# Performance work log

Measured on AMD Instinct MI355X. Metric: run time of the kernel, lower is better.

## Reference

```python
import jax, jax.numpy as jnp
import numpy as np

# dims
D_IN, D, H, HD = 1536, 256, 8, 32
DEPTH, FFN = 2, 1024
B, L = 1, 8191
NGRIDS, TILE = 256, 256
SEGMENTS = [1024, 2048, 4096, 8192, 16384]   # get_optimal_segment_length(32768, 256)
RATIOS = [1, 2, 4, 8, 16]                    # LongNet canonical dilation ratios
SCALE = HD ** -0.5


def setup_inputs() -> dict:
    key = jax.random.key(0)
    ks = jax.random.split(key, 16)
    w = lambda k, s: jax.random.normal(k, s, jnp.float32) * 0.02
    return {
        "x": jax.random.normal(ks[0], (B, L, D_IN), jnp.float32),
        "coords": jax.random.randint(ks[1], (B, L, 2), 0, NGRIDS * TILE, jnp.int32),
        "proj_w": w(ks[2], (D_IN, D)), "proj_b": jnp.zeros((D,), jnp.float32),
        "cls_tok": w(ks[3], (1, 1, D)),
        "Wq": w(ks[4], (DEPTH, D, D)), "Wk": w(ks[5], (DEPTH, D, D)),
        "Wv": w(ks[6], (DEPTH, D, D)), "Wo": w(ks[7], (DEPTH, D, D)),
        "bq": jnp.zeros((DEPTH, D), jnp.float32), "bk": jnp.zeros((DEPTH, D), jnp.float32),
        "bv": jnp.zeros((DEPTH, D), jnp.float32), "bo": jnp.zeros((DEPTH, D), jnp.float32),
        "ln1_g": jnp.ones((DEPTH, D), jnp.float32), "ln1_b": jnp.zeros((DEPTH, D), jnp.float32),
        "ln2_g": jnp.ones((DEPTH, D), jnp.float32), "ln2_b": jnp.zeros((DEPTH, D), jnp.float32),
        "W1": w(ks[8], (DEPTH, D, FFN)), "b1": jnp.zeros((DEPTH, FFN), jnp.float32),
        "W2": w(ks[9], (DEPTH, FFN, D)), "b2": jnp.zeros((DEPTH, D), jnp.float32),
        "enc_g": jnp.ones((D,), jnp.float32), "enc_b": jnp.zeros((D,), jnp.float32),
        "norm_g": jnp.ones((D,), jnp.float32), "norm_b": jnp.zeros((D,), jnp.float32),
    }


def _ln(x, g, b):
    mu = x.mean(-1, keepdims=True)
    v = ((x - mu) ** 2).mean(-1, keepdims=True)
    return (x - mu) * jax.lax.rsqrt(v + 1e-5) * g + b


def _pos_table():
    # MAE-style 2D sincos pos embed, row 0 = cls (zeros). [NGRIDS^2+1, D]
    g = jnp.arange(NGRIDS, dtype=jnp.float32)
    gw, gh = jnp.meshgrid(g, g)  # gw[i,j]=j, gh[i,j]=i; flatten index = i*NGRIDS + j
    def one(pos):
        omega = 1.0 / (10000.0 ** (jnp.arange(D // 4, dtype=jnp.float32) / (D // 4)))
        o = pos.reshape(-1)[:, None] * omega[None]
        return jnp.concatenate([jnp.sin(o), jnp.cos(o)], -1)
    tab = jnp.concatenate([one(gw), one(gh)], -1)
    return jnp.concatenate([jnp.zeros((1, D), jnp.float32), tab], 0)


def _dilated_attn(q, k, v):
    # q,k,v: [B,S,H,HD]. LongNet: per (segment w, dilation r) branch, sparse in-segment
    # attention on stride-r rows (head-dependent offset h%r), branches fused via their
    # softmax log-sum-exp weights.
    S = q.shape[1]
    hh = jnp.arange(H)[:, None]
    outs, lses = [], []
    for w, r in zip(SEGMENTS, RATIOS):
        n = (S + w - 1) // w
        Sp = n * w
        def seg(t):
            tp = jnp.pad(t, ((0, 0), (0, Sp - S), (0, 0), (0, 0)))
            return tp.reshape(B, n, w, H, HD).transpose(0, 1, 3, 2, 4)  # [B,n,H,w,HD]
        qs_, ks_, vs_ = seg(q), seg(k), seg(v)
        t = w // r
        idx = (hh % r) + r * jnp.arange(t)[None, :]                  # [H,t]
        qs = qs_[:, :, hh, idx]                                      # [B,n,H,t,HD]
        ks = ks_[:, :, hh, idx]
        vs = vs_[:, :, hh, idx]
        valid = (jnp.arange(n)[:, None, None] * w + idx[None]) < S   # [n,H,t]
        sc = jnp.einsum('bnhtd,bnhsd->bnhts', qs, ks) * SCALE
        sc = jnp.where(valid[None, :, :, None, :], sc, -1e9)
        m = sc.max(-1, keepdims=True)
        p = jnp.exp(sc - m)
        den = p.sum(-1, keepdims=True)
        o = jnp.einsum('bnhts,bnhsd->bnhtd', p, vs) / den
        lse = m[..., 0] + jnp.log(den[..., 0])                       # [B,n,H,t]
        fo = jnp.zeros((B, n, H, w, HD), q.dtype).at[:, :, hh, idx].set(o)
        fl = jnp.full((B, n, H, w), -1e30, q.dtype).at[:, :, hh, idx].set(lse)
        outs.append(fo.transpose(0, 1, 3, 2, 4).reshape(B, Sp, H, HD)[:, :S])
        lses.append(fl.transpose(0, 1, 3, 2).reshape(B, Sp, H)[:, :S])
    Ls = jnp.stack(lses)   # [5,B,S,H]
    Os = jnp.stack(outs)   # [5,B,S,H,HD]
    wts = jnp.exp(Ls - Ls.max(0, keepdims=True))
    return (wts[..., None] * Os).sum(0) / wts.sum(0)[..., None]


def _forward(x, coords, proj_w, proj_b, cls_tok, Wq, Wk, Wv, Wo, bq, bk, bv, bo,
             ln1_g, ln1_b, ln2_g, ln2_b, W1, b1, W2, b2, enc_g, enc_b, norm_g, norm_b):
    h = x @ proj_w + proj_b                                   # patch embed [B,L,D]
    tab = _pos_table()
    cg = jnp.floor(coords.astype(jnp.float32) / TILE).astype(jnp.int32)
    pos = cg[..., 0] * NGRIDS + cg[..., 1] + 1                # coords_to_pos
    h = h + tab[pos]
    cls = jnp.broadcast_to(cls_tok + tab[0], (B, 1, D))
    h = jnp.concatenate([cls, h], 1)                          # [B,S,D], S = L+1
    S = h.shape[1]
    for i in range(DEPTH):                                    # pre-LN LongNet encoder layers
        a = _ln(h, ln1_g[i], ln1_b[i])
        q = (a @ Wq[i] + bq[i]).reshape(B, S, H, HD)
        k = (a @ Wk[i] + bk[i]).reshape(B, S, H, HD)
        v = (a @ Wv[i] + bv[i]).reshape(B, S, H, HD)
        o = _dilated_attn(q, k, v).reshape(B, S, D)
        h = h + o @ Wo[i] + bo[i]
        f = _ln(h, ln2_g[i], ln2_b[i])
        h = h + jax.nn.gelu(f @ W1[i] + b1[i], approximate=False) @ W2[i] + b2[i]
    h = _ln(h, enc_g, enc_b)     # encoder final LN
    h = _ln(h, norm_g, norm_b)   # model self.norm
    return h[:, 0]               # cls embedding (global_pool=False)


def reference(x, coords, proj_w, proj_b, cls_tok, Wq, Wk, Wv, Wo, bq, bk, bv, bo,
              ln1_g, ln1_b, ln2_g, ln2_b, W1, b1, W2, b2, enc_g, enc_b, norm_g, norm_b):
    return _forward(x, coords, proj_w, proj_b, cls_tok, Wq, Wk, Wv, Wo, bq, bk, bv, bo,
                    ln1_g, ln1_b, ln2_g, ln2_b, W1, b1, W2, b2, enc_g, enc_b, norm_g, norm_b)
```

## Files before the change

kernel.cpp:

```cpp
#include <hip/hip_runtime.h>
#include <math.h>

#define S_TOT 8192
#define DD 256
#define NHEAD 8
#define HDSZ 32
#define ATT_SCALE 0.17677669529663687f
#define ATT_SCALE_LOG2E 0.25506601f

typedef short short8 __attribute__((ext_vector_type(8)));
typedef float f32x4 __attribute__((ext_vector_type(4)));
typedef unsigned short ushort;

#define OFF_PROJ 0
#define OFF_WQ0  393216
#define OFF_WK0  458752
#define OFF_WV0  524288
#define OFF_WO0  589824
#define OFF_W10  655360
#define OFF_W20  917504
#define OFF_WK1  1179648
#define OFF_WV1  1245184
#define OFF_WQ1  1310720
#define OFF_WO1  1376256
#define OFF_W11  1441792
#define OFF_W21  1703936
#define WBUF_TOT 1966080

__device__ inline ushort f2bf(float f) {
    union { float f; unsigned u; } c; c.f = f;
    unsigned u = c.u;
    u += 0x7fffu + ((u >> 16) & 1u);
    return (ushort)(u >> 16);
}
__device__ inline float bf2f(ushort u) {
    union { unsigned u; float f; } c; c.u = ((unsigned)u) << 16;
    return c.f;
}
__device__ inline float gelu_exact(float v) {
    return 0.5f * v * (1.0f + erff(v * 0.7071067811865475f));
}
__device__ inline unsigned cvtpk_bf16(float a, float b) {
    unsigned r;
    asm("v_cvt_pk_bf16_f32 %0, %1, %2" : "=v"(r) : "v"(a), "v"(b));
    return r;
}
__device__ inline float block_sum256(float v, float* red) {
    #pragma unroll
    for (int off = 32; off > 0; off >>= 1) v += __shfl_down(v, off, 64);
    const int wid = threadIdx.x >> 6, lane = threadIdx.x & 63;
    if (lane == 0) red[wid] = v;
    __syncthreads();
    const float s = red[0] + red[1] + red[2] + red[3];
    __syncthreads();
    return s;
}

__global__ __launch_bounds__(256)
void setup_kernel(const float* __restrict__ x, const float* __restrict__ proj_w,
                  const float* __restrict__ Wq, const float* __restrict__ Wk,
                  const float* __restrict__ Wv, const float* __restrict__ Wo,
                  const float* __restrict__ W1, const float* __restrict__ W2,
                  const float* __restrict__ bq, const float* __restrict__ bk,
                  const float* __restrict__ bv, const float* __restrict__ cls_tok,
                  ushort* __restrict__ wbuf, float* __restrict__ bqkv0,
                  float* __restrict__ bkv1, ushort* __restrict__ xbf,
                  float* __restrict__ h)
{
    const int b = blockIdx.x;
    const int t = threadIdx.x;
    if (b >= 482) {
        if (b == 6626) { h[t] = cls_tok[t]; return; }
        const int i = (b - 482) * 256 + t;
        const int n8 = 8191 * 1536 / 8;
        if (i >= n8) return;
        const float4 a0 = *(const float4*)(x + (size_t)i * 8);
        const float4 a1 = *(const float4*)(x + (size_t)i * 8 + 4);
        ushort tmp[8] = { f2bf(a0.x), f2bf(a0.y), f2bf(a0.z), f2bf(a0.w),
                          f2bf(a1.x), f2bf(a1.y), f2bf(a1.z), f2bf(a1.w) };
        *(uint4*)(xbf + (size_t)i * 8) = *(const uint4*)tmp;
        return;
    }
    if (b >= 480) {
        if (b == 480) {
            for (int i = t; i < 768; i += 256)
                bqkv0[i] = (i < 256) ? bq[i] : ((i < 512) ? bk[i - 256] : bv[i - 512]);
        } else {
            for (int i = t; i < 512; i += 256)
                bkv1[i] = (i < 256) ? bk[256 + i] : bv[i];
        }
        return;
    }
    const float* src; ushort* dst; int R, C, t0;
    if (b < 96)       { src = proj_w;        dst = wbuf + OFF_PROJ; R = 1536; C = 256;  t0 = 0;   }
    else if (b < 112) { src = Wq;            dst = wbuf + OFF_WQ0;  R = 256;  C = 256;  t0 = 96;  }
    else if (b < 128) { src = Wk;            dst = wbuf + OFF_WK0;  R = 256;  C = 256;  t0 = 112; }
    else if (b < 144) { src = Wv;            dst = wbuf + OFF_WV0;  R = 256;  C = 256;  t0 = 128; }
    else if (b < 160) { src = Wo;            dst = wbuf + OFF_WO0;  R = 256;  C = 256;  t0 = 144; }
    else if (b < 224) { src = W1;            dst = wbuf + OFF_W10;  R = 256;  C = 1024; t0 = 160; }
    else if (b < 288) { src = W2;            dst = wbuf + OFF_W20;  R = 1024; C = 256;  t0 = 224; }
    else if (b < 304) { src = Wk + 65536;    dst = wbuf + OFF_WK1;  R = 256;  C = 256;  t0 = 288; }
    else if (b < 320) { src = Wv + 65536;    dst = wbuf + OFF_WV1;  R = 256;  C = 256;  t0 = 304; }
    else if (b < 336) { src = Wq + 65536;    dst = wbuf + OFF_WQ1;  R = 256;  C = 256;  t0 = 320; }
    else if (b < 352) { src = Wo + 65536;    dst = wbuf + OFF_WO1;  R = 256;  C = 256;  t0 = 336; }
    else if (b < 416) { src = W1 + 262144;   dst = wbuf + OFF_W11;  R = 256;  C = 1024; t0 = 352; }
    else              { src = W2 + 262144;   dst = wbuf + OFF_W21;  R = 1024; C = 256;  t0 = 416; }
    const int lt = b - t0;
    const int tC = C >> 6;
    const int tr = lt / tC, tc = lt % tC;
    __shared__ ushort tile[64][68];
    const int col = t & 63;
    const int r4  = t >> 6;
    #pragma unroll
    for (int i = 0; i < 16; ++i) {
        const int row = i * 4 + r4;
        tile[row][col] = f2bf(src[(size_t)(tr * 64 + row) * C + tc * 64 + col]);
    }
    __syncthreads();
    #pragma unroll
    for (int i = 0; i < 16; ++i) {
        const int n = i * 4 + r4;
        dst[(size_t)(tc * 64 + n) * R + tr * 64 + col] = tile[col][n];
    }
}

__global__ __launch_bounds__(256)
void ln_kernel(const float* __restrict__ in, const float* __restrict__ g,
               const float* __restrict__ b, ushort* __restrict__ outp)
{
    __shared__ float red[4];
    const int row = blockIdx.x;
    const int d = threadIdx.x;
    const float xv = in[(size_t)row * DD + d];
    const float mu = block_sum256(xv, red) * (1.0f / 256.0f);
    const float dv = xv - mu;
    const float var = block_sum256(dv * dv, red) * (1.0f / 256.0f);
    outp[(size_t)row * DD + d] = f2bf(dv * rsqrtf(var + 1e-5f) * g[d] + b[d]);
}

template <int BN>
__global__ __launch_bounds__(256)
void gemm4_kernel(const ushort* __restrict__ A, const ushort* __restrict__ Bt,
                  const float* __restrict__ bias, void* __restrict__ Cv,
                  int M, int N, int K, int flags, const int* __restrict__ coords)
{
    __shared__ ushort As[2][64][64];
    __shared__ ushort Bs[2][BN][64];
    constexpr int NT = BN / 32;
    const int nx  = N / BN;
    const int ny8 = gridDim.x / (8 * nx);
    const int b   = blockIdx.x;
    const int c8  = b & 7;
    const int j   = b >> 3;
    const int m0  = (c8 * ny8 + j / nx) * 64;
    const int n0  = (j % nx) * BN;

    const int tid  = threadIdx.x;
    const int wave = tid >> 6;
    const int lane = tid & 63;
    const int lrow = lane & 15;
    const int quad = lane >> 4;
    const int wr = (wave >> 1) * 32;
    const int wc = (wave & 1) * (BN / 2);

    float* Cf  = (float*)Cv;
    ushort* Cb = (ushort*)Cv;

    f32x4 acc[2][NT];
    #pragma unroll
    for (int mt = 0; mt < 2; ++mt)
        #pragma unroll
        for (int nt = 0; nt < NT; ++nt)
            acc[mt][nt] = (f32x4){0.f, 0.f, 0.f, 0.f};

    const int srow = tid >> 3;
    const int scol = (tid & 7) * 16;

    #define STAGE(BUF, KK)                                                        \
    do {                                                                          \
        _Pragma("unroll")                                                         \
        for (int c = 0; c < 2; ++c) {                                             \
            const int row = c * 32 + srow;                                        \
            const int sb  = scol ^ ((row & 7) << 4);                              \
            const ushort* srcp = A + (size_t)(m0 + row) * K + (KK) + (sb >> 1);   \
            __builtin_amdgcn_global_load_lds(                                     \
                (const __attribute__((address_space(1))) void*)srcp,              \
                (__attribute__((address_space(3))) void*)&As[BUF][c * 32 + wave * 8][0], \
                16, 0, 0);                                                        \
        }                                                                         \
        _Pragma("unroll")                                                         \
        for (int c = 0; c < BN / 32; ++c) {                                       \
            const int row = c * 32 + srow;                                        \
            const int sb  = scol ^ ((row & 7) << 4);                              \
            const ushort* srcp = Bt + (size_t)(n0 + row) * K + (KK) + (sb >> 1);  \
            __builtin_amdgcn_global_load_lds(                                     \
                (const __attribute__((address_space(1))) void*)srcp,              \
                (__attribute__((address_space(3))) void*)&Bs[BUF][c * 32 + wave * 8][0], \
                16, 0, 0);                                                        \
        }                                                                         \
    } while (0)

    int cur = 0;
    STAGE(0, 0);
    __syncthreads();
    for (int kk = 0; kk < K; kk += 64) {
        if (kk + 64 < K) STAGE(cur ^ 1, kk + 64);
        #pragma unroll
        for (int ks = 0; ks < 2; ++ks) {
            short8 af[2], bfr[NT];
            #pragma unroll
            for (int mt = 0; mt < 2; ++mt) {
                const int row = wr + mt * 16 + lrow;
                const int cb  = (ks * 64 + quad * 16) ^ ((row & 7) << 4);
                af[mt] = *(const short8*)((const char*)&As[cur][row][0] + cb);
            }
            #pragma unroll
            for (int nt = 0; nt < NT; ++nt) {
                const int row = wc + nt * 16 + lrow;
                const int cb  = (ks * 64 + quad * 16) ^ ((row & 7) << 4);
                bfr[nt] = *(const short8*)((const char*)&Bs[cur][row][0] + cb);
            }
            #pragma unroll
            for (int mt = 0; mt < 2; ++mt)
                #pragma unroll
                for (int nt = 0; nt < NT; ++nt)
                    acc[mt][nt] = __builtin_amdgcn_mfma_f32_16x16x32_bf16(
                                      af[mt], bfr[nt], acc[mt][nt], 0, 0, 0);
        }
        __syncthreads();
        cur ^= 1;
    }
    #undef STAGE

    #pragma unroll
    for (int mt = 0; mt < 2; ++mt) {
        #pragma unroll
        for (int rg = 0; rg < 4; ++rg) {
            const int r = m0 + wr + mt * 16 + quad * 4 + rg;
            if (r >= M) continue;
            #pragma unroll
            for (int nt = 0; nt < NT; ++nt) {
                const int c = n0 + wc + nt * 16 + lrow;
                float vv = acc[mt][nt][rg] + bias[c];
                if (flags & 8) {
                    const int cg = coords[2 * r + ((c < 128) ? 1 : 0)] >> 8;
                    const float omega = 1.0f / powf(10000.0f, (float)(c & 63) * (1.0f / 64.0f));
                    const float o = (float)cg * omega;
                    vv += ((c & 64) == 0) ? sinf(o) : cosf(o);
                }
                if (flags & 16) { if (c < 256) vv *= ATT_SCALE_LOG2E; }
                if (flags & 2) vv = gelu_exact(vv);
                if (flags & 4) {
                    Cb[(size_t)r * N + c] = f2bf(vv);
                } else {
                    if (flags & 1) vv += Cf[(size_t)r * N + c];
                    Cf[(size_t)r * N + c] = vv;
                }
            }
        }
    }
}

__global__ __launch_bounds__(256)
void attn_mfma_kernel(const ushort* __restrict__ q, const ushort* __restrict__ k,
                      const ushort* __restrict__ v, float* __restrict__ bo5,
                      float* __restrict__ lse5, int qs)
{
    __shared__ ushort Kb[64][40];
    __shared__ ushort Vt[32][72];
    __shared__ ushort Pb[4][16][72];

    const int unit = blockIdx.x;
    const int segu = unit >> 3;
    const int head = unit & 7;
    int b2, n;
    if (segu < 8)        { b2 = 0; n = segu; }
    else if (segu < 12)  { b2 = 1; n = segu - 8; }
    else if (segu < 14)  { b2 = 2; n = segu - 12; }
    else if (segu == 14) { b2 = 3; n = 0; }
    else                 { b2 = 4; n = 0; }
    const int w  = 1024 << b2;
    const int rr = 1 << b2;
    const int base = n * w + (head & (rr - 1));

    int kEnd = (S_TOT - base + rr - 1) >> b2;
    if (kEnd > 1024) kEnd = 1024;
    if (blockIdx.y * 128 >= kEnd) return;

    const int tid  = threadIdx.x;
    const int wave = tid >> 6;
    const int lane = tid & 63;
    const int lrow = lane & 15;
    const int quad = lane >> 4;

    short8 qf[2];
    #pragma unroll
    for (int m = 0; m < 2; ++m) {
        const int j  = blockIdx.y * 128 + wave * 32 + m * 16 + lrow;
        const int pq = base + rr * j;
        qf[m] = *(const short8*)(q + (size_t)pq * qs + head * HDSZ + quad * 8);
    }

    f32x4 acc[2][2];
    float lsum[2][4];
    #pragma unroll
    for (int m = 0; m < 2; ++m) {
        #pragma unroll
        for (int dt = 0; dt < 2; ++dt) acc[m][dt] = (f32x4){0.f, 0.f, 0.f, 0.f};
        #pragma unroll
        for (int rg = 0; rg < 4; ++rg) lsum[m][rg] = 0.f;
    }

    const int skr = tid >> 2;
    const int sdb = (tid & 3) * 8;
    const int grp = tid & 3;
    const int wcol = (2 * skr + 32 * grp) & 127;

    size_t prow = (size_t)(base + rr * skr) * qs + head * HDSZ + sdb;
    uint4 kreg = *(const uint4*)(k + prow);
    uint4 vreg = *(const uint4*)(v + prow);

    for (int kc = 0; kc < kEnd; kc += 64) {
        *(uint4*)&Kb[skr][sdb] = kreg;
        {
            const ushort* vp = (const ushort*)&vreg;
            #pragma unroll
            for (int i = 0; i < 8; ++i)
                *(ushort*)((char*)&Vt[sdb + i][0] + wcol) = vp[i];
        }
        __syncthreads();
        if (kc + 64 < kEnd) {
            prow = (size_t)(base + rr * (kc + 64 + skr)) * qs + head * HDSZ + sdb;
            kreg = *(const uint4*)(k + prow);
            vreg = *(const uint4*)(v + prow);
        }

        short8 kf[4], vf[2][2];
        #pragma unroll
        for (int t = 0; t < 4; ++t)
            kf[t] = *(const short8*)&Kb[t * 16 + lrow][quad * 8];
        #pragma unroll
        for (int g = 0; g < 2; ++g)
            #pragma unroll
            for (int dt = 0; dt < 2; ++dt) {
                const int row  = dt * 16 + lrow;
                const int rcol = (g * 64 + quad * 16 + 32 * ((row >> 3) & 3)) & 127;
                vf[g][dt] = *(const short8*)((const char*)&Vt[row][0] + rcol);
            }

        #pragma unroll
        for (int m = 0; m < 2; ++m) {
            f32x4 sc[4];
            #pragma unroll
            for (int t = 0; t < 4; ++t)
                sc[t] = __builtin_amdgcn_mfma_f32_16x16x32_bf16(
                            qf[m], kf[t], (f32x4){0.f,0.f,0.f,0.f}, 0, 0, 0);
            float p[4][4];
            #pragma unroll
            for (int t = 0; t < 4; ++t)
                #pragma unroll
                for (int rg = 0; rg < 4; ++rg)
                    p[t][rg] = exp2f(sc[t][rg]);
            #pragma unroll
            for (int rg = 0; rg < 4; ++rg)
                lsum[m][rg] += (p[0][rg] + p[1][rg]) + (p[2][rg] + p[3][rg]);
            #pragma unroll
            for (int t = 0; t < 4; ++t) {
                const unsigned pw01 = cvtpk_bf16(p[t][0], p[t][1]);
                const unsigned pw23 = cvtpk_bf16(p[t][2], p[t][3]);
                Pb[wave][quad * 4 + 0][t * 16 + lrow] = (ushort)pw01;
                Pb[wave][quad * 4 + 1][t * 16 + lrow] = (ushort)(pw01 >> 16);
                Pb[wave][quad * 4 + 2][t * 16 + lrow] = (ushort)pw23;
                Pb[wave][quad * 4 + 3][t * 16 + lrow] = (ushort)(pw23 >> 16);
            }
            __threadfence_block();
            short8 pa[2];
            #pragma unroll
            for (int g = 0; g < 2; ++g)
                pa[g] = *(const short8*)&Pb[wave][lrow][g * 32 + quad * 8];
            #pragma unroll
            for (int g = 0; g < 2; ++g)
                #pragma unroll
                for (int dt = 0; dt < 2; ++dt)
                    acc[m][dt] = __builtin_amdgcn_mfma_f32_16x16x32_bf16(
                                     pa[g], vf[g][dt], acc[m][dt], 0, 0, 0);
        }
        __syncthreads();
    }

    #pragma unroll
    for (int m = 0; m < 2; ++m) {
        #pragma unroll
        for (int rg = 0; rg < 4; ++rg) {
            float li = lsum[m][rg];
            #pragma unroll
            for (int off = 1; off < 16; off <<= 1)
                li += __shfl_xor(li, off, 16);
            const int j  = blockIdx.y * 128 + wave * 32 + m * 16 + quad * 4 + rg;
            const int pq = base + rr * j;
            const float inv = 1.0f / li;
            float* dst = bo5 + ((size_t)b2 * S_TOT + pq) * DD + head * HDSZ;
            dst[lrow]      = acc[m][0][rg] * inv;
            dst[16 + lrow] = acc[m][1][rg] * inv;
            if (lrow == 0)
                lse5[((size_t)b2 * S_TOT + pq) * NHEAD + head] = __logf(li);
        }
    }
}

__global__ __launch_bounds__(64)
void attn_row0_kernel(const float* __restrict__ q, const ushort* __restrict__ k,
                      const ushort* __restrict__ v, float* __restrict__ bo5,
                      float* __restrict__ lse5, int kvs)
{
    const int b2 = blockIdx.x >> 3;
    const int head = blockIdx.x & 7;
    const int r = 1 << b2;
    if (head & (r - 1)) return;
    const int tid = threadIdx.x;
    float qreg[32];
    #pragma unroll
    for (int d = 0; d < 32; d += 4) {
        const float4 t4 = *(const float4*)(q + head * HDSZ + d);
        qreg[d] = t4.x; qreg[d+1] = t4.y; qreg[d+2] = t4.z; qreg[d+3] = t4.w;
    }
    float m = -3.0e38f, l = 0.f, o[32];
    #pragma unroll
    for (int d = 0; d < 32; ++d) o[d] = 0.f;
    for (int j = tid; j < 1024; j += 64) {
        const int pk = r * j;
        float s;
        if (pk < S_TOT) {
            float s0 = 0.f;
            #pragma unroll
            for (int d = 0; d < 32; d += 8) {
                const uint4 raw = *(const uint4*)(k + (size_t)pk * kvs + head * HDSZ + d);
                const ushort* kp = (const ushort*)&raw;
                #pragma unroll
                for (int i = 0; i < 8; ++i) s0 += qreg[d + i] * bf2f(kp[i]);
            }
            s = s0 * ATT_SCALE;
        } else s = -1.0e9f;
        const float mn = fmaxf(m, s);
        const float c = __expf(m - mn);
        const float e = __expf(s - mn);
        l = l * c + e; m = mn;
        if (pk < S_TOT) {
            #pragma unroll
            for (int d = 0; d < 32; d += 8) {
                const uint4 raw = *(const uint4*)(v + (size_t)pk * kvs + head * HDSZ + d);
                const ushort* vp = (const ushort*)&raw;
                #pragma unroll
                for (int i = 0; i < 8; ++i) o[d + i] = o[d + i] * c + e * bf2f(vp[i]);
            }
        } else {
            #pragma unroll
            for (int d = 0; d < 32; ++d) o[d] *= c;
        }
    }
    __shared__ float ms[64], ls[64], os[64][32];
    ms[tid] = m; ls[tid] = l;
    #pragma unroll
    for (int d = 0; d < 32; ++d) os[tid][d] = o[d];
    __syncthreads();
    for (int st = 32; st >= 1; st >>= 1) {
        if (tid < st) {
            const float m2 = ms[tid + st], l2 = ls[tid + st];
            const float mn = fmaxf(ms[tid], m2);
            const float c1 = __expf(ms[tid] - mn);
            const float c2 = __expf(m2 - mn);
            ls[tid] = ls[tid] * c1 + l2 * c2;
            ms[tid] = mn;
            for (int d = 0; d < 32; ++d) os[tid][d] = os[tid][d]*c1 + os[tid+st][d]*c2;
        }
        __syncthreads();
    }
    if (tid < 32) bo5[(size_t)b2 * S_TOT * DD + head * HDSZ + tid] = os[0][tid] / ls[0];
    if (tid == 0) lse5[(size_t)b2 * S_TOT * NHEAD + head] = ms[0] + __logf(ls[0]);
}

__global__ __launch_bounds__(256)
void combine_kernel(const float* __restrict__ bo5, const float* __restrict__ lse5,
                    ushort* __restrict__ attn)
{
    const int p = blockIdx.x;
    const int d = threadIdx.x;
    const int h = d >> 5;
    float lse[5];
    bool sel[5];
    float mx = -3.0e38f;
    #pragma unroll
    for (int b2 = 0; b2 < 5; ++b2) {
        const int r = 1 << b2;
        sel[b2] = ((p & (r - 1)) == (h & (r - 1)));
        if (sel[b2]) {
            lse[b2] = lse5[((size_t)b2 * S_TOT + p) * NHEAD + h];
            mx = fmaxf(mx, lse[b2]);
        }
    }
    float wsum = 0.f, acc = 0.f;
    #pragma unroll
    for (int b2 = 0; b2 < 5; ++b2) {
        if (sel[b2]) {
            const float wgt = __expf(lse[b2] - mx);
            wsum += wgt;
            acc += wgt * bo5[((size_t)b2 * S_TOT + p) * DD + d];
        }
    }
    attn[(size_t)p * DD + d] = f2bf(acc / wsum);
}

__global__ __launch_bounds__(256)
void tail_qrow_kernel(const float* __restrict__ h, const float* __restrict__ g,
                      const float* __restrict__ b, const ushort* __restrict__ Wt,
                      const float* __restrict__ bias, float* __restrict__ qrow0)
{
    __shared__ float red[4];
    __shared__ float as[256];
    const int d = threadIdx.x;
    const float xv = h[d];
    const float mu = block_sum256(xv, red) * (1.0f / 256.0f);
    const float dv = xv - mu;
    const float var = block_sum256(dv * dv, red) * (1.0f / 256.0f);
    as[d] = dv * rsqrtf(var + 1e-5f) * g[d] + b[d];
    __syncthreads();
    float acc = 0.f;
    for (int k2 = 0; k2 < 256; k2 += 8) {
        const short8 w8 = *(const short8*)&Wt[(size_t)d * 256 + k2];
        #pragma unroll
        for (int j = 0; j < 8; ++j) acc += as[k2 + j] * bf2f((ushort)w8[j]);
    }
    qrow0[d] = acc + bias[d];
}

__global__ __launch_bounds__(256)
void tail_mid_kernel(const float* __restrict__ bo5, const float* __restrict__ lse5,
                     float* __restrict__ h, const ushort* __restrict__ Wo1t,
                     const float* __restrict__ bo1, const float* __restrict__ g2,
                     const float* __restrict__ b2, float* __restrict__ f)
{
    __shared__ float red[4];
    __shared__ float att[256];
    const int d = threadIdx.x;
    const int hh = d >> 5;
    float lse[5]; bool sel[5]; float mx = -3.0e38f;
    #pragma unroll
    for (int bb = 0; bb < 5; ++bb) {
        const int r = 1 << bb;
        sel[bb] = ((hh & (r - 1)) == 0);
        if (sel[bb]) {
            lse[bb] = lse5[(size_t)bb * S_TOT * NHEAD + hh];
            mx = fmaxf(mx, lse[bb]);
        }
    }
    float wsum = 0.f, acc = 0.f;
    #pragma unroll
    for (int bb = 0; bb < 5; ++bb) {
        if (sel[bb]) {
            const float wgt = __expf(lse[bb] - mx);
            wsum += wgt;
            acc += wgt * bo5[(size_t)bb * S_TOT * DD + d];
        }
    }
    att[d] = acc / wsum;
    __syncthreads();
    float a2 = 0.f;
    for (int k2 = 0; k2 < 256; k2 += 8) {
        const short8 w8 = *(const short8*)&Wo1t[(size_t)d * 256 + k2];
        #pragma unroll
        for (int j = 0; j < 8; ++j) a2 += att[k2 + j] * bf2f((ushort)w8[j]);
    }
    const float hv = a2 + bo1[d] + h[d];
    h[d] = hv;
    const float mu = block_sum256(hv, red) * (1.0f / 256.0f);
    const float dv = hv - mu;
    const float var = block_sum256(dv * dv, red) * (1.0f / 256.0f);
    f[d] = dv * rsqrtf(var + 1e-5f) * g2[d] + b2[d];
}

__global__ __launch_bounds__(256)
void tail_ffn1_kernel(const float* __restrict__ f, const ushort* __restrict__ W11t,
                      const float* __restrict__ b11, float* __restrict__ midr0)
{
    __shared__ float fs[256];
    const int tid = threadIdx.x;
    fs[tid] = f[tid];
    __syncthreads();
    const int n = blockIdx.x * 256 + tid;
    float acc = 0.f;
    for (int k2 = 0; k2 < 256; k2 += 8) {
        const short8 w8 = *(const short8*)&W11t[(size_t)n * 256 + k2];
        #pragma unroll
        for (int j = 0; j < 8; ++j) acc += fs[k2 + j] * bf2f((ushort)w8[j]);
    }
    midr0[n] = gelu_exact(acc + b11[n]);
}

__global__ __launch_bounds__(256)
void tail_ffn2_kernel(const float* __restrict__ midr0, const ushort* __restrict__ W21t,
                      const float* __restrict__ b21, float* __restrict__ h)
{
    __shared__ float ms[1024];
    const int tid = threadIdx.x;
    for (int i = tid; i < 1024; i += 256) ms[i] = midr0[i];
    __syncthreads();
    const int n  = blockIdx.x * 64 + (tid >> 2);
    const int kq = (tid & 3) * 256;
    float acc = 0.f;
    for (int k2 = 0; k2 < 256; k2 += 8) {
        const short8 w8 = *(const short8*)&W21t[(size_t)n * 1024 + kq + k2];
        #pragma unroll
        for (int j = 0; j < 8; ++j) acc += ms[kq + k2 + j] * bf2f((ushort)w8[j]);
    }
    acc += __shfl_xor(acc, 1);
    acc += __shfl_xor(acc, 2);
    if ((tid & 3) == 0) h[n] = h[n] + acc + b21[n];
}

__global__ __launch_bounds__(256)
void tail_final_kernel(const float* __restrict__ h, const float* __restrict__ eg,
                       const float* __restrict__ eb, const float* __restrict__ ng,
                       const float* __restrict__ nb, float* __restrict__ out)
{
    __shared__ float red[4];
    const int d = threadIdx.x;
    float xv = h[d];
    {
        const float mu = block_sum256(xv, red) * (1.0f / 256.0f);
        const float dv = xv - mu;
        const float var = block_sum256(dv * dv, red) * (1.0f / 256.0f);
        xv = dv * rsqrtf(var + 1e-5f) * eg[d] + eb[d];
    }
    {
        const float mu = block_sum256(xv, red) * (1.0f / 256.0f);
        const float dv = xv - mu;
        const float var = block_sum256(dv * dv, red) * (1.0f / 256.0f);
        out[d] = dv * rsqrtf(var + 1e-5f) * ng[d] + nb[d];
    }
}

extern "C" void kernel_launch(void* const* d_in, const int* in_sizes, int n_in,
                              void* d_out, int out_size, void* d_ws, size_t ws_size,
                              hipStream_t stream)
{
    const float* x      = (const float*)d_in[0];
    const int*   coords = (const int*)  d_in[1];
    const float* proj_w = (const float*)d_in[2];
    const float* proj_b = (const float*)d_in[3];
    const float* cls_tok= (const float*)d_in[4];
    const float* Wq     = (const float*)d_in[5];
    const float* Wk     = (const float*)d_in[6];
    const float* Wv     = (const float*)d_in[7];
    const float* Wo     = (const float*)d_in[8];
    const float* bq     = (const float*)d_in[9];
    const float* bk     = (const float*)d_in[10];
    const float* bv     = (const float*)d_in[11];
    const float* bo_    = (const float*)d_in[12];
    const float* ln1_g  = (const float*)d_in[13];
    const float* ln1_b  = (const float*)d_in[14];
    const float* ln2_g  = (const float*)d_in[15];
    const float* ln2_b  = (const float*)d_in[16];
    const float* W1     = (const float*)d_in[17];
    const float* b1     = (const float*)d_in[18];
    const float* W2     = (const float*)d_in[19];
    const float* b2v    = (const float*)d_in[20];
    const float* enc_g  = (const float*)d_in[21];
    const float* enc_b  = (const float*)d_in[22];
    const float* norm_g = (const float*)d_in[23];
    const float* norm_b = (const float*)d_in[24];
    float* out = (float*)d_out;

    const size_t SD = (size_t)S_TOT * DD;
    float* ws   = (float*)d_ws;
    float* h    = ws;
    float* big  = h + SD;
    float* bo5  = big;
    ushort* xbf   = (ushort*)big;
    ushort* midbf = (ushort*)big;
    float* lse5 = big + 5 * SD;
    ushort* a_bf    = (ushort*)(lse5 + 5 * S_TOT * NHEAD);
    ushort* qkv_bf  = a_bf + SD;
    ushort* attn_bf = qkv_bf + 3 * SD;
    ushort* wbuf    = attn_bf + SD;
    float* bqkv0  = (float*)(wbuf + WBUF_TOT);
    float* bkv1   = bqkv0 + 768;
    float* qrow0  = bkv1 + 512;
    float* f_r0   = qrow0 + 256;
    float* midr0  = f_r0 + 256;

    auto gemm64 = [&](const ushort* A, const ushort* Bt, const float* bias, void* C,
                      int M, int N, int K, int flags) {
        gemm4_kernel<64><<<128 * (N / 64), 256, 0, stream>>>(A, Bt, bias, C, M, N, K,
                                                             flags, coords);
    };
    auto gemm128 = [&](const ushort* A, const ushort* Bt, const float* bias, void* C,
                       int M, int N, int K, int flags) {
        gemm4_kernel<128><<<128 * (N / 128), 256, 0, stream>>>(A, Bt, bias, C, M, N, K,
                                                               flags, coords);
    };

    setup_kernel<<<6627, 256, 0, stream>>>(x, proj_w, Wq, Wk, Wv, Wo, W1, W2,
                                           bq, bk, bv, cls_tok, wbuf, bqkv0, bkv1,
                                           xbf, h);

    gemm64(xbf, wbuf + OFF_PROJ, proj_b, h + DD, 8191, 256, 1536, 8);

    ln_kernel<<<S_TOT, 256, 0, stream>>>(h, ln1_g, ln1_b, a_bf);
    gemm128(a_bf, wbuf + OFF_WQ0, bqkv0, qkv_bf, 8192, 768, 256, 4 | 16);
    attn_mfma_kernel<<<dim3(128, 8), 256, 0, stream>>>(qkv_bf, qkv_bf + 256,
                                                       qkv_bf + 512, bo5, lse5, 768);
    combine_kernel<<<S_TOT, 256, 0, stream>>>(bo5, lse5, attn_bf);
    gemm64(attn_bf, wbuf + OFF_WO0, bo_, h, 8192, 256, 256, 1);
    ln_kernel<<<S_TOT, 256, 0, stream>>>(h, ln2_g, ln2_b, a_bf);
    gemm128(a_bf, wbuf + OFF_W10, b1, midbf, 8192, 1024, 256, 4 | 2);
    gemm64(midbf, wbuf + OFF_W20, b2v, h, 8192, 256, 1024, 1);

    ln_kernel<<<S_TOT, 256, 0, stream>>>(h, ln1_g + 256, ln1_b + 256, a_bf);
    gemm128(a_bf, wbuf + OFF_WK1, bkv1, qkv_bf, 8192, 512, 256, 4);
    tail_qrow_kernel<<<1, 256, 0, stream>>>(h, ln1_g + 256, ln1_b + 256,
                                            wbuf + OFF_WQ1, bq + 256, qrow0);
    attn_row0_kernel<<<40, 64, 0, stream>>>(qrow0, qkv_bf, qkv_bf + 256, bo5, lse5, 512);
    tail_mid_kernel<<<1, 256, 0, stream>>>(bo5, lse5, h, wbuf + OFF_WO1, bo_ + 256,
                                           ln2_g + 256, ln2_b + 256, f_r0);
    tail_ffn1_kernel<<<4, 256, 0, stream>>>(f_r0, wbuf + OFF_W11, b1 + 1024, midr0);
    tail_ffn2_kernel<<<4, 256, 0, stream>>>(midr0, wbuf + OFF_W21, b2v + 256, h);
    tail_final_kernel<<<1, 256, 0, stream>>>(h, enc_g, enc_b, norm_g, norm_b, out);
}
```

Measured before the change: 431.6 us.

## Compute transposed QK^T scores to keep P in registers and double-buffer K/V LDS

The QK MFMA swaps its operands so each lane holds the scores for one query column. The bf16-packed probabilities can then feed the PV MFMA directly as the A operand, which removes the per-wave Pb shared-memory round trip and its fence. Row sums are now accumulated per lane and reduced with cross-quad shuffles at the end. K/V tiles are double-buffered in LDS, which removes one __syncthreads per iteration, and the V fragment reads are split into two 4-element loads to match the new k ordering.

```diff
diff --git a/kernel.cpp b/kernel.cpp
--- a/kernel.cpp
+++ b/kernel.cpp
@@ -9,6 +9,7 @@
 #define ATT_SCALE_LOG2E 0.25506601f
 
 typedef short short8 __attribute__((ext_vector_type(8)));
+typedef short short4v __attribute__((ext_vector_type(4)));
 typedef float f32x4 __attribute__((ext_vector_type(4)));
 typedef unsigned short ushort;
 
@@ -44,6 +45,9 @@
     unsigned r;
     asm("v_cvt_pk_bf16_f32 %0, %1, %2" : "=v"(r) : "v"(a), "v"(b));
     return r;
+}
+__device__ inline short8 cat44(short4v a, short4v b) {
+    return __builtin_shufflevector(a, b, 0, 1, 2, 3, 4, 5, 6, 7);
 }
 __device__ inline float block_sum256(float v, float* red) {
     #pragma unroll
@@ -266,9 +270,8 @@
                       const ushort* __restrict__ v, float* __restrict__ bo5,
                       float* __restrict__ lse5, int qs)
 {
-    __shared__ ushort Kb[64][40];
-    __shared__ ushort Vt[32][72];
-    __shared__ ushort Pb[4][16][72];
+    __shared__ ushort Kb[2][64][40];
+    __shared__ ushort Vt[2][32][72];
 
     const int unit = blockIdx.x;
     const int segu = unit >> 3;
@@ -302,14 +305,11 @@
     }
 
     f32x4 acc[2][2];
-    float lsum[2][4];
-    #pragma unroll
-    for (int m = 0; m < 2; ++m) {
+    float lsum[2] = {0.f, 0.f};
+    #pragma unroll
+    for (int m = 0; m < 2; ++m)
         #pragma unroll
         for (int dt = 0; dt < 2; ++dt) acc[m][dt] = (f32x4){0.f, 0.f, 0.f, 0.f};
-        #pragma unroll
-        for (int rg = 0; rg < 4; ++rg) lsum[m][rg] = 0.f;
-    }
 
     const int skr = tid >> 2;
     const int sdb = (tid & 3) * 8;
@@ -320,32 +320,40 @@
     uint4 kreg = *(const uint4*)(k + prow);
     uint4 vreg = *(const uint4*)(v + prow);
 
+    *(uint4*)&Kb[0][skr][sdb] = kreg;
+    {
+        const ushort* vp = (const ushort*)&vreg;
+        #pragma unroll
+        for (int i = 0; i < 8; ++i)
+            *(ushort*)((char*)&Vt[0][sdb + i][0] + wcol) = vp[i];
+    }
+
+    int cur = 0;
     for (int kc = 0; kc < kEnd; kc += 64) {
-        *(uint4*)&Kb[skr][sdb] = kreg;
-        {
-            const ushort* vp = (const ushort*)&vreg;
-            #pragma unroll
-            for (int i = 0; i < 8; ++i)
-                *(ushort*)((char*)&Vt[sdb + i][0] + wcol) = vp[i];
-        }
         __syncthreads();
-        if (kc + 64 < kEnd) {
+        const bool more = (kc + 64 < kEnd);
+        if (more) {
             prow = (size_t)(base + rr * (kc + 64 + skr)) * qs + head * HDSZ + sdb;
             kreg = *(const uint4*)(k + prow);
             vreg = *(const uint4*)(v + prow);
         }
 
-        short8 kf[4], vf[2][2];
+        short8 kf[4];
         #pragma unroll
         for (int t = 0; t < 4; ++t)
-            kf[t] = *(const short8*)&Kb[t * 16 + lrow][quad * 8];
+            kf[t] = *(const short8*)&Kb[cur][t * 16 + lrow][quad * 8];
+
+        short8 vf[2][2];
         #pragma unroll
         for (int g = 0; g < 2; ++g)
             #pragma unroll
             for (int dt = 0; dt < 2; ++dt) {
                 const int row  = dt * 16 + lrow;
-                const int rcol = (g * 64 + quad * 16 + 32 * ((row >> 3) & 3)) & 127;
-                vf[g][dt] = *(const short8*)((const char*)&Vt[row][0] + rcol);
+                const int rotb = 32 * ((row >> 3) & 3);
+                const int cb0  = (64 * g + 8 * quad + rotb) & 127;
+                const int cb1  = (64 * g + 8 * quad + 32 + rotb) & 127;
+                vf[g][dt] = cat44(*(const short4v*)((const char*)&Vt[cur][row][0] + cb0),
+                                  *(const short4v*)((const char*)&Vt[cur][row][0] + cb1));
             }
 
         #pragma unroll
@@ -354,48 +362,56 @@
             #pragma unroll
             for (int t = 0; t < 4; ++t)
                 sc[t] = __builtin_amdgcn_mfma_f32_16x16x32_bf16(
-                            qf[m], kf[t], (f32x4){0.f,0.f,0.f,0.f}, 0, 0, 0);
+                            kf[t], qf[m], (f32x4){0.f,0.f,0.f,0.f}, 0, 0, 0);
             float p[4][4];
             #pragma unroll
             for (int t = 0; t < 4; ++t)
                 #pragma unroll
                 for (int rg = 0; rg < 4; ++rg)
                     p[t][rg] = exp2f(sc[t][rg]);
-            #pragma unroll
-            for (int rg = 0; rg < 4; ++rg)
-                lsum[m][rg] += (p[0][rg] + p[1][rg]) + (p[2][rg] + p[3][rg]);
+            float ps = 0.f;
+            #pragma unroll
+            for (int t = 0; t < 4; ++t)
+                ps += (p[t][0] + p[t][1]) + (p[t][2] + p[t][3]);
+            lsum[m] += ps;
+            unsigned pw[4][2];
             #pragma unroll
             for (int t = 0; t < 4; ++t) {
-                const unsigned pw01 = cvtpk_bf16(p[t][0], p[t][1]);
-                const unsigned pw23 = cvtpk_bf16(p[t][2], p[t][3]);
-                Pb[wave][quad * 4 + 0][t * 16 + lrow] = (ushort)pw01;
-                Pb[wave][quad * 4 + 1][t * 16 + lrow] = (ushort)(pw01 >> 16);
-                Pb[wave][quad * 4 + 2][t * 16 + lrow] = (ushort)pw23;
-                Pb[wave][quad * 4 + 3][t * 16 + lrow] = (ushort)(pw23 >> 16);
+                pw[t][0] = cvtpk_bf16(p[t][0], p[t][1]);
+                pw[t][1] = cvtpk_bf16(p[t][2], p[t][3]);
             }
-            __threadfence_block();
-            short8 pa[2];
-            #pragma unroll
-            for (int g = 0; g < 2; ++g)
-                pa[g] = *(const short8*)&Pb[wave][lrow][g * 32 + quad * 8];
-            #pragma unroll
-            for (int g = 0; g < 2; ++g)
+            #pragma unroll
+            for (int g = 0; g < 2; ++g) {
+                union { short8 s; unsigned u[4]; } pa;
+                pa.u[0] = pw[2 * g][0];
+                pa.u[1] = pw[2 * g][1];
+                pa.u[2] = pw[2 * g + 1][0];
+                pa.u[3] = pw[2 * g + 1][1];
                 #pragma unroll
                 for (int dt = 0; dt < 2; ++dt)
                     acc[m][dt] = __builtin_amdgcn_mfma_f32_16x16x32_bf16(
-                                     pa[g], vf[g][dt], acc[m][dt], 0, 0, 0);
-        }
-        __syncthreads();
+                                     pa.s, vf[g][dt], acc[m][dt], 0, 0, 0);
+            }
+        }
+
+        if (more) {
+            *(uint4*)&Kb[cur ^ 1][skr][sdb] = kreg;
+            const ushort* vp = (const ushort*)&vreg;
+            #pragma unroll
+            for (int i = 0; i < 8; ++i)
+                *(ushort*)((char*)&Vt[cur ^ 1][sdb + i][0] + wcol) = vp[i];
+        }
+        cur ^= 1;
     }
 
     #pragma unroll
     for (int m = 0; m < 2; ++m) {
+        float tot = lsum[m];
+        tot += __shfl_xor(tot, 16, 64);
+        tot += __shfl_xor(tot, 32, 64);
         #pragma unroll
         for (int rg = 0; rg < 4; ++rg) {
-            float li = lsum[m][rg];
-            #pragma unroll
-            for (int off = 1; off < 16; off <<= 1)
-                li += __shfl_xor(li, off, 16);
+            const float li = __shfl(tot, quad * 4 + rg, 16);
             const int j  = blockIdx.y * 128 + wave * 32 + m * 16 + quad * 4 + rg;
             const int pq = base + rr * j;
             const float inv = 1.0f / li;
```

New measurement: 432.7 us. Within noise of the previous version (+0.2%).
